# Kernel optimization log

Measured on AMD Instinct MI355X. Metric: run time of the kernel, lower is better.

## Reference

```python
import jax, jax.numpy as jnp
import numpy as np

B, L, D = 4, 8192, 1024

def setup_inputs() -> dict:
    key = jax.random.key(0)
    kx, kg, kc = jax.random.split(key, 3)
    scale = 1.0 / np.sqrt(D)  # ~xavier for [D,D]
    return {
        "x": jax.random.normal(kx, (B, L, D), dtype=jnp.float32),
        "Wg": jax.random.normal(kg, (D, D), dtype=jnp.float32) * scale,
        "bg": jnp.ones((D,), dtype=jnp.float32),   # gate bias init = 1.0
        "Wc": jax.random.normal(kc, (D, D), dtype=jnp.float32) * scale,
        "bc": jnp.zeros((D,), dtype=jnp.float32),  # candidate bias init = 0
    }

def _mingru_scan(gates, candidates):
    # Linear recurrence h_t = g_t * h_{t-1} + c_t, h_0 = 0, along axis=1 (L).
    # Associative combine for pairs (a, b) representing h -> a*h + b.
    def combine(e1, e2):
        a1, b1 = e1
        a2, b2 = e2
        return a2 * a1, a2 * b1 + b2
    _, h = jax.lax.associative_scan(combine, (gates, candidates), axis=1)
    return h

def reference(x, Wg, bg, Wc, bc):
    # gate_proj / candidate_proj: y = x @ W.T + b (torch Linear convention)
    gates = jax.nn.sigmoid(jnp.einsum('bld,ed->ble', x, Wg) + bg)
    candidates = jnp.tanh(jnp.einsum('bld,ed->ble', x, Wc) + bc)
    return _mingru_scan(gates, candidates)  # dropout=0 -> identity
```

## Files before the change

### kernel.cpp

```cpp
#include <hip/hip_runtime.h>
#include <math.h>

#define B_ 4
#define L_ 8192
#define D_ 1024
#define M_ (B_ * L_)
#define K_ D_

#define BM 128
#define BN 128
#define BK 32

#define NC 128
#define CHUNK (L_ / NC)

typedef short bf16x8 __attribute__((ext_vector_type(8)));
typedef float f32x4 __attribute__((ext_vector_type(4)));

__device__ __forceinline__ unsigned short f2bf(float f) {
    unsigned u = __float_as_uint(f);
    u += 0x7fff + ((u >> 16) & 1);
    return (unsigned short)(u >> 16);
}
__device__ __forceinline__ float bf2f(unsigned short h) {
    return __uint_as_float(((unsigned)h) << 16);
}

__device__ __forceinline__ void async16(const void* g, void* l) {
    __builtin_amdgcn_global_load_lds(
        (const __attribute__((address_space(1))) unsigned int*)g,
        (__attribute__((address_space(3))) unsigned int*)l, 16, 0, 0);
}

__global__ __launch_bounds__(256) void wprep_kernel(
    const float* __restrict__ Wg, const float* __restrict__ Wc,
    unsigned short* __restrict__ Wghi, unsigned short* __restrict__ Wglo,
    unsigned short* __restrict__ Wchi, unsigned short* __restrict__ Wclo)
{
    int idx = (blockIdx.x * 256 + threadIdx.x) * 4;
    const int n = D_ * D_;
    const float* src; unsigned short *dh, *dl; int o;
    if (idx < n) { src = Wg; dh = Wghi; dl = Wglo; o = idx; }
    else         { src = Wc; dh = Wchi; dl = Wclo; o = idx - n; }
    float4 v = *(const float4*)(src + o);
    ushort4 hi, lo;
    hi.x = f2bf(v.x); lo.x = f2bf(v.x - bf2f(hi.x));
    hi.y = f2bf(v.y); lo.y = f2bf(v.y - bf2f(hi.y));
    hi.z = f2bf(v.z); lo.z = f2bf(v.z - bf2f(hi.z));
    hi.w = f2bf(v.w); lo.w = f2bf(v.w - bf2f(hi.w));
    *(ushort4*)(dh + o) = hi;
    *(ushort4*)(dl + o) = lo;
}

__global__ __launch_bounds__(256) void gemm_mfma_kernel(
    const float* __restrict__ X,
    const unsigned short* __restrict__ Wghi, const unsigned short* __restrict__ Wglo,
    const unsigned short* __restrict__ Wchi, const unsigned short* __restrict__ Wclo,
    const float* __restrict__ bg, const float* __restrict__ bc,
    float* __restrict__ g_ws, float* __restrict__ c_ws)
{
    __shared__ __align__(16) unsigned short sAhi[BM * BK];
    __shared__ __align__(16) unsigned short sAlo[BM * BK];
    __shared__ __align__(16) unsigned short sBhi[BN * BK];
    __shared__ __align__(16) unsigned short sBlo[BN * BK];

    const int t = threadIdx.x;
    const int lane = t & 63;
    const int w = t >> 6;
    const int wrow = w >> 1;
    const int wcol = w & 1;
    const int quad = lane >> 4;
    const int l16  = lane & 15;

    const int mblk = blockIdx.x;
    const int nblk = blockIdx.y;
    const bool isGate = (nblk < 8);
    const unsigned short* __restrict__ Whi = isGate ? Wghi : Wchi;
    const unsigned short* __restrict__ Wlo = isGate ? Wglo : Wclo;
    const float* __restrict__ bias = isGate ? bg : bc;
    float* __restrict__ outp       = isGate ? g_ws : c_ws;
    const int n0 = (nblk & 7) * BN;
    const int m0 = mblk * BM;

    f32x4 acc[4][4] = {};

#pragma unroll 1
    for (int k0 = 0; k0 < K_; k0 += BK) {
        __syncthreads();

#pragma unroll
        for (int p = 0; p < 2; ++p) {
            int o   = t * 16 + p * 4096;
            int row = o >> 6;
            int kc  = (o & 63) >> 1;
            const unsigned short* srcH = Whi + (size_t)(n0 + row) * K_ + k0 + kc;
            const unsigned short* srcL = Wlo + (size_t)(n0 + row) * K_ + k0 + kc;
            async16(srcH, (char*)sBhi + o);
            async16(srcL, (char*)sBlo + o);
        }

#pragma unroll
        for (int p = 0; p < 4; ++p) {
            int idx = (p * 256 + t) * 4;
            int row = idx >> 5;
            int k   = idx & 31;
            float4 v = *(const float4*)(X + (size_t)(m0 + row) * K_ + k0 + k);
            ushort4 hi, lo;
            hi.x = f2bf(v.x); lo.x = f2bf(v.x - bf2f(hi.x));
            hi.y = f2bf(v.y); lo.y = f2bf(v.y - bf2f(hi.y));
            hi.z = f2bf(v.z); lo.z = f2bf(v.z - bf2f(hi.z));
            hi.w = f2bf(v.w); lo.w = f2bf(v.w - bf2f(hi.w));
            *(ushort4*)(sAhi + row * BK + k) = hi;
            *(ushort4*)(sAlo + row * BK + k) = lo;
        }

        __syncthreads();

        bf16x8 ahi[4], alo[4];
#pragma unroll
        for (int i = 0; i < 4; ++i) {
            int off = (wrow * 64 + i * 16 + l16) * BK + quad * 8;
            ahi[i] = *(const bf16x8*)(sAhi + off);
            alo[i] = *(const bf16x8*)(sAlo + off);
        }
#pragma unroll
        for (int j = 0; j < 4; ++j) {
            int off = (wcol * 64 + j * 16 + l16) * BK + quad * 8;
            bf16x8 bhi = *(const bf16x8*)(sBhi + off);
            bf16x8 blo = *(const bf16x8*)(sBlo + off);
#pragma unroll
            for (int i = 0; i < 4; ++i) {
                acc[i][j] = __builtin_amdgcn_mfma_f32_16x16x32_bf16(ahi[i], bhi, acc[i][j], 0, 0, 0);
                acc[i][j] = __builtin_amdgcn_mfma_f32_16x16x32_bf16(ahi[i], blo, acc[i][j], 0, 0, 0);
                acc[i][j] = __builtin_amdgcn_mfma_f32_16x16x32_bf16(alo[i], bhi, acc[i][j], 0, 0, 0);
            }
        }
    }

#pragma unroll
    for (int j = 0; j < 4; ++j) {
        int n = n0 + wcol * 64 + j * 16 + l16;
        float bv = bias[n];
#pragma unroll
        for (int i = 0; i < 4; ++i) {
#pragma unroll
            for (int r = 0; r < 4; ++r) {
                int m = m0 + wrow * 64 + i * 16 + quad * 4 + r;
                float z = acc[i][j][r] + bv;
                float vv = isGate ? (1.f / (1.f + __expf(-z))) : tanhf(z);
                outp[(size_t)m * D_ + n] = vv;
            }
        }
    }
}

__global__ __launch_bounds__(256) void scan_phase1(
    const float* __restrict__ g_ws, const float* __restrict__ c_ws,
    float* __restrict__ carryA, float* __restrict__ carryB)
{
    const int t = threadIdx.x;
    const int cid = blockIdx.x;
    const int b   = blockIdx.y;
    const size_t base = ((size_t)b * L_ + (size_t)cid * CHUNK) * D_;
    const float4* g4 = (const float4*)(g_ws + base) + t;
    const float4* c4 = (const float4*)(c_ws + base) + t;

    float4 A  = make_float4(1.f, 1.f, 1.f, 1.f);
    float4 Bv = make_float4(0.f, 0.f, 0.f, 0.f);
#pragma unroll 4
    for (int l = 0; l < CHUNK; ++l) {
        float4 g = g4[(size_t)l * (D_ / 4)];
        float4 c = c4[(size_t)l * (D_ / 4)];
        Bv.x = fmaf(g.x, Bv.x, c.x); Bv.y = fmaf(g.y, Bv.y, c.y);
        Bv.z = fmaf(g.z, Bv.z, c.z); Bv.w = fmaf(g.w, Bv.w, c.w);
        A.x *= g.x; A.y *= g.y; A.z *= g.z; A.w *= g.w;
    }
    const size_t cbase = ((size_t)b * NC + cid) * D_;
    ((float4*)(carryA + cbase))[t] = A;
    ((float4*)(carryB + cbase))[t] = Bv;
}

__global__ __launch_bounds__(256) void scan_phase2(
    const float* __restrict__ carryA, float* __restrict__ carryB)
{
    const int idx = blockIdx.x * 256 + threadIdx.x;
    const int b = idx >> 10;
    const int d = idx & (D_ - 1);
    float accB = 0.f;
    for (int k = 0; k < NC; ++k) {
        const size_t o = ((size_t)b * NC + k) * D_ + d;
        const float a  = carryA[o];
        const float bb = carryB[o];
        carryB[o] = accB;
        accB = fmaf(a, accB, bb);
    }
}

__global__ __launch_bounds__(256) void scan_phase3(
    const float* __restrict__ g_ws, const float* __restrict__ c_ws,
    const float* __restrict__ carryB, float* __restrict__ out)
{
    const int t = threadIdx.x;
    const int cid = blockIdx.x;
    const int b   = blockIdx.y;
    const size_t base = ((size_t)b * L_ + (size_t)cid * CHUNK) * D_;
    const float4* g4 = (const float4*)(g_ws + base) + t;
    const float4* c4 = (const float4*)(c_ws + base) + t;
    float4* o4 = (float4*)(out + base) + t;

    const size_t cbase = ((size_t)b * NC + cid) * D_;
    float4 h = ((const float4*)(carryB + cbase))[t];
#pragma unroll 4
    for (int l = 0; l < CHUNK; ++l) {
        float4 g = g4[(size_t)l * (D_ / 4)];
        float4 c = c4[(size_t)l * (D_ / 4)];
        h.x = fmaf(g.x, h.x, c.x); h.y = fmaf(g.y, h.y, c.y);
        h.z = fmaf(g.z, h.z, c.z); h.w = fmaf(g.w, h.w, c.w);
        o4[(size_t)l * (D_ / 4)] = h;
    }
}

extern "C" void kernel_launch(void* const* d_in, const int* in_sizes, int n_in,
                              void* d_out, int out_size, void* d_ws, size_t ws_size,
                              hipStream_t stream)
{
    const float* x  = (const float*)d_in[0];
    const float* Wg = (const float*)d_in[1];
    const float* bg = (const float*)d_in[2];
    const float* Wc = (const float*)d_in[3];
    const float* bc = (const float*)d_in[4];
    float* out = (float*)d_out;

    float* ws = (float*)d_ws;
    float* g_ws   = ws;
    float* c_ws   = g_ws + (size_t)M_ * D_;
    float* carryA = c_ws + (size_t)M_ * D_;
    float* carryB = carryA + (size_t)B_ * NC * D_;
    unsigned short* Wghi = (unsigned short*)(carryB + (size_t)B_ * NC * D_);
    unsigned short* Wglo = Wghi + (size_t)D_ * D_;
    unsigned short* Wchi = Wglo + (size_t)D_ * D_;
    unsigned short* Wclo = Wchi + (size_t)D_ * D_;

    wprep_kernel<<<(2 * D_ * D_ / 4) / 256, 256, 0, stream>>>(
        Wg, Wc, Wghi, Wglo, Wchi, Wclo);

    dim3 ggrid(M_ / BM, 16);
    gemm_mfma_kernel<<<ggrid, 256, 0, stream>>>(
        x, Wghi, Wglo, Wchi, Wclo, bg, bc, g_ws, c_ws);

    scan_phase1<<<dim3(NC, B_), 256, 0, stream>>>(g_ws, c_ws, carryA, carryB);
    scan_phase2<<<(B_ * D_) / 256, 256, 0, stream>>>(carryA, carryB);
    scan_phase3<<<dim3(NC, B_), 256, 0, stream>>>(g_ws, c_ws, carryB, out);
}
```

Measured before the change: 837.6 us.

## Pre-split X into bf16 hi/lo globally and async-load A tiles; reuse output as gate buffer

Adds a separate pass that converts X once into bf16 hi/lo arrays, so the GEMM loads A tiles with async global-to-LDS copies instead of converting fp32 in registers for each of the 16 N-blocks. The gate buffer is now the output array itself, which removes one M×D fp32 workspace and lets phase 3 overwrite gates in place. It also adds a separate carry output and unrolls the phase-2 loop. The trade-off is an extra full read of X plus a write of two bf16 copies, against removing sixteen-fold redundant conversion work inside the GEMM.

```diff
diff --git a/kernel.cpp b/kernel.cpp
--- a/kernel.cpp
+++ b/kernel.cpp
@@ -52,12 +52,27 @@
     *(ushort4*)(dl + o) = lo;
 }
 
+__global__ __launch_bounds__(256) void xsplit_kernel(
+    const float* __restrict__ X,
+    unsigned short* __restrict__ Xhi, unsigned short* __restrict__ Xlo)
+{
+    size_t idx = ((size_t)blockIdx.x * 256 + threadIdx.x) * 4;
+    float4 v = *(const float4*)(X + idx);
+    ushort4 hi, lo;
+    hi.x = f2bf(v.x); lo.x = f2bf(v.x - bf2f(hi.x));
+    hi.y = f2bf(v.y); lo.y = f2bf(v.y - bf2f(hi.y));
+    hi.z = f2bf(v.z); lo.z = f2bf(v.z - bf2f(hi.z));
+    hi.w = f2bf(v.w); lo.w = f2bf(v.w - bf2f(hi.w));
+    *(ushort4*)(Xhi + idx) = hi;
+    *(ushort4*)(Xlo + idx) = lo;
+}
+
 __global__ __launch_bounds__(256) void gemm_mfma_kernel(
-    const float* __restrict__ X,
+    const unsigned short* __restrict__ Xhi, const unsigned short* __restrict__ Xlo,
     const unsigned short* __restrict__ Wghi, const unsigned short* __restrict__ Wglo,
     const unsigned short* __restrict__ Wchi, const unsigned short* __restrict__ Wclo,
     const float* __restrict__ bg, const float* __restrict__ bc,
-    float* __restrict__ g_ws, float* __restrict__ c_ws)
+    float* __restrict__ g_out, float* __restrict__ c_ws)
 {
     __shared__ __align__(16) unsigned short sAhi[BM * BK];
     __shared__ __align__(16) unsigned short sAlo[BM * BK];
@@ -78,7 +93,7 @@
     const unsigned short* __restrict__ Whi = isGate ? Wghi : Wchi;
     const unsigned short* __restrict__ Wlo = isGate ? Wglo : Wclo;
     const float* __restrict__ bias = isGate ? bg : bc;
-    float* __restrict__ outp       = isGate ? g_ws : c_ws;
+    float* __restrict__ outp       = isGate ? g_out : c_ws;
     const int n0 = (nblk & 7) * BN;
     const int m0 = mblk * BM;
 
@@ -93,25 +108,12 @@
             int o   = t * 16 + p * 4096;
             int row = o >> 6;
             int kc  = (o & 63) >> 1;
-            const unsigned short* srcH = Whi + (size_t)(n0 + row) * K_ + k0 + kc;
-            const unsigned short* srcL = Wlo + (size_t)(n0 + row) * K_ + k0 + kc;
-            async16(srcH, (char*)sBhi + o);
-            async16(srcL, (char*)sBlo + o);
-        }
-
-#pragma unroll
-        for (int p = 0; p < 4; ++p) {
-            int idx = (p * 256 + t) * 4;
-            int row = idx >> 5;
-            int k   = idx & 31;
-            float4 v = *(const float4*)(X + (size_t)(m0 + row) * K_ + k0 + k);
-            ushort4 hi, lo;
-            hi.x = f2bf(v.x); lo.x = f2bf(v.x - bf2f(hi.x));
-            hi.y = f2bf(v.y); lo.y = f2bf(v.y - bf2f(hi.y));
-            hi.z = f2bf(v.z); lo.z = f2bf(v.z - bf2f(hi.z));
-            hi.w = f2bf(v.w); lo.w = f2bf(v.w - bf2f(hi.w));
-            *(ushort4*)(sAhi + row * BK + k) = hi;
-            *(ushort4*)(sAlo + row * BK + k) = lo;
+            size_t aoff = (size_t)(m0 + row) * K_ + k0 + kc;
+            size_t boff = (size_t)(n0 + row) * K_ + k0 + kc;
+            async16(Xhi + aoff, (char*)sAhi + o);
+            async16(Xlo + aoff, (char*)sAlo + o);
+            async16(Whi + boff, (char*)sBhi + o);
+            async16(Wlo + boff, (char*)sBlo + o);
         }
 
         __syncthreads();
@@ -181,42 +183,43 @@
 }
 
 __global__ __launch_bounds__(256) void scan_phase2(
-    const float* __restrict__ carryA, float* __restrict__ carryB)
+    const float* __restrict__ carryA, const float* __restrict__ carryB,
+    float* __restrict__ carryC)
 {
     const int idx = blockIdx.x * 256 + threadIdx.x;
     const int b = idx >> 10;
     const int d = idx & (D_ - 1);
     float accB = 0.f;
+#pragma unroll 8
     for (int k = 0; k < NC; ++k) {
         const size_t o = ((size_t)b * NC + k) * D_ + d;
         const float a  = carryA[o];
         const float bb = carryB[o];
-        carryB[o] = accB;
+        carryC[o] = accB;
         accB = fmaf(a, accB, bb);
     }
 }
 
 __global__ __launch_bounds__(256) void scan_phase3(
-    const float* __restrict__ g_ws, const float* __restrict__ c_ws,
-    const float* __restrict__ carryB, float* __restrict__ out)
+    const float* __restrict__ c_ws, const float* __restrict__ carryC,
+    float* __restrict__ gout)
 {
     const int t = threadIdx.x;
     const int cid = blockIdx.x;
     const int b   = blockIdx.y;
     const size_t base = ((size_t)b * L_ + (size_t)cid * CHUNK) * D_;
-    const float4* g4 = (const float4*)(g_ws + base) + t;
     const float4* c4 = (const float4*)(c_ws + base) + t;
-    float4* o4 = (float4*)(out + base) + t;
+    float4* go4 = (float4*)(gout + base) + t;
 
     const size_t cbase = ((size_t)b * NC + cid) * D_;
-    float4 h = ((const float4*)(carryB + cbase))[t];
+    float4 h = ((const float4*)(carryC + cbase))[t];
 #pragma unroll 4
     for (int l = 0; l < CHUNK; ++l) {
-        float4 g = g4[(size_t)l * (D_ / 4)];
+        float4 g = go4[(size_t)l * (D_ / 4)];
         float4 c = c4[(size_t)l * (D_ / 4)];
         h.x = fmaf(g.x, h.x, c.x); h.y = fmaf(g.y, h.y, c.y);
         h.z = fmaf(g.z, h.z, c.z); h.w = fmaf(g.w, h.w, c.w);
-        o4[(size_t)l * (D_ / 4)] = h;
+        go4[(size_t)l * (D_ / 4)] = h;
     }
 }
 
@@ -232,23 +235,26 @@
     float* out = (float*)d_out;
 
     float* ws = (float*)d_ws;
-    float* g_ws   = ws;
-    float* c_ws   = g_ws + (size_t)M_ * D_;
+    float* c_ws   = ws;
     float* carryA = c_ws + (size_t)M_ * D_;
     float* carryB = carryA + (size_t)B_ * NC * D_;
     unsigned short* Wghi = (unsigned short*)(carryB + (size_t)B_ * NC * D_);
     unsigned short* Wglo = Wghi + (size_t)D_ * D_;
     unsigned short* Wchi = Wglo + (size_t)D_ * D_;
     unsigned short* Wclo = Wchi + (size_t)D_ * D_;
+    unsigned short* Xhi  = Wclo + (size_t)D_ * D_;
+    unsigned short* Xlo  = Xhi + (size_t)M_ * D_;
+    float* carryC = (float*)Xhi;
 
     wprep_kernel<<<(2 * D_ * D_ / 4) / 256, 256, 0, stream>>>(
         Wg, Wc, Wghi, Wglo, Wchi, Wclo);
+    xsplit_kernel<<<((size_t)M_ * D_ / 4) / 256, 256, 0, stream>>>(x, Xhi, Xlo);
 
     dim3 ggrid(M_ / BM, 16);
     gemm_mfma_kernel<<<ggrid, 256, 0, stream>>>(
-        x, Wghi, Wglo, Wchi, Wclo, bg, bc, g_ws, c_ws);
-
-    scan_phase1<<<dim3(NC, B_), 256, 0, stream>>>(g_ws, c_ws, carryA, carryB);
-    scan_phase2<<<(B_ * D_) / 256, 256, 0, stream>>>(carryA, carryB);
-    scan_phase3<<<dim3(NC, B_), 256, 0, stream>>>(g_ws, c_ws, carryB, out);
-}
+        Xhi, Xlo, Wghi, Wglo, Wchi, Wclo, bg, bc, out, c_ws);
+
+    scan_phase1<<<dim3(NC, B_), 256, 0, stream>>>(out, c_ws, carryA, carryB);
+    scan_phase2<<<(B_ * D_) / 256, 256, 0, stream>>>(carryA, carryB, carryC);
+    scan_phase3<<<dim3(NC, B_), 256, 0, stream>>>(c_ws, carryC, out);
+}
```

Result: slower. 912.9 us (+9.0%).
